# Kernel optimization log

Measured on AMD Instinct MI355X. Metric: run time of the kernel, lower is better.

Reference implementation:

```python
import jax, jax.numpy as jnp
import numpy as np
from jax import lax

G, K, C_IN, C_FEAT, H, W, B = 8, 6, 512, 256, 64, 64, 1


def apply_offset(offset):
    # offset: [N, 2, H, W] pixel-space offsets -> sampling grid [N, H, W, 2] in [-1, 1]
    # channel 0 displaces x (width), channel 1 displaces y (height), matching the
    # reversed-meshgrid logic of the original torch apply_offset.
    n, _, h, w = offset.shape
    jj = jnp.arange(w, dtype=offset.dtype)[None, None, :]
    ii = jnp.arange(h, dtype=offset.dtype)[None, :, None]
    gx = (jj + offset[:, 0]) / ((w - 1.0) / 2.0) - 1.0
    gy = (ii + offset[:, 1]) / ((h - 1.0) / 2.0) - 1.0
    return jnp.stack([gx, gy], axis=-1)


def grid_sample_border(img, grid):
    # img: [N, C, H, W], grid: [N, H, W, 2] in [-1, 1]
    # Bilinear, padding_mode='border', align_corners=False (torch grid_sample default).
    n, c, h, w = img.shape
    x = jnp.clip((grid[..., 0] + 1.0) * w * 0.5 - 0.5, 0.0, w - 1.0)
    y = jnp.clip((grid[..., 1] + 1.0) * h * 0.5 - 0.5, 0.0, h - 1.0)
    x0 = jnp.floor(x)
    y0 = jnp.floor(y)
    wx = (x - x0)[:, None]  # [N,1,H,W]
    wy = (y - y0)[:, None]
    x0i = x0.astype(jnp.int32)
    y0i = y0.astype(jnp.int32)
    x1i = jnp.minimum(x0i + 1, w - 1)
    y1i = jnp.minimum(y0i + 1, h - 1)

    def gather(im, yi, xi):  # im [C,H,W]; yi, xi [H,W]
        return im[:, yi, xi]

    g = jax.vmap(gather)
    v00 = g(img, y0i, x0i)
    v01 = g(img, y0i, x1i)
    v10 = g(img, y1i, x0i)
    v11 = g(img, y1i, x1i)
    return (1.0 - wy) * ((1.0 - wx) * v00 + wx * v01) + wy * ((1.0 - wx) * v10 + wx * v11)


def setup_inputs() -> dict:
    key = jax.random.key(0)
    ks = jax.random.split(key, 11)
    s = 0.02
    return {
        "gar_feat": jax.random.normal(ks[0], (B, C_FEAT, H, W), jnp.float32),
        "cond_feat": jax.random.normal(ks[1], (B, C_FEAT, H, W), jnp.float32),
        "mask": jax.random.uniform(ks[2], (B, G, C_FEAT), dtype=jnp.float32),
        "W1": jax.random.normal(ks[3], (G, 128, C_IN, 3, 3), jnp.float32) * s,
        "b1": jax.random.normal(ks[4], (G, 128), jnp.float32) * s,
        "W2": jax.random.normal(ks[5], (G, 64, 128, 3, 3), jnp.float32) * s,
        "b2": jax.random.normal(ks[6], (G, 64), jnp.float32) * s,
        "W3": jax.random.normal(ks[7], (G, 32, 64, 3, 3), jnp.float32) * s,
        "b3": jax.random.normal(ks[8], (G, 32), jnp.float32) * s,
        "W4": jax.random.normal(ks[9], (G, 3 * K, 32, 3, 3), jnp.float32) * s,
        "b4": jax.random.normal(ks[10], (G, 3 * K), jnp.float32) * s,
    }


def reference(gar_feat, cond_feat, mask, W1, b1, W2, b2, W3, b3, W4, b4):
    b, c, h, w = gar_feat.shape
    g = W1.shape[0]
    k = W4.shape[1] // 3
    inp = jnp.concatenate([gar_feat, cond_feat], axis=1)  # [B, 2C, H, W]

    def conv(x, wgt, bias):
        return lax.conv_general_dilated(
            x, wgt, (1, 1), 'SAME', dimension_numbers=('NCHW', 'OIHW', 'NCHW')
        ) + bias[None, :, None, None]

    def lrelu(x):
        return jnp.where(x >= 0, x, 0.1 * x)

    def group_net(w1, bb1, w2, bb2, w3, bb3, w4, bb4):
        hid = lrelu(conv(inp, w1, bb1))
        hid = lrelu(conv(hid, w2, bb2))
        hid = lrelu(conv(hid, w3, bb3))
        return conv(hid, w4, bb4)  # [B, 3k, H, W]

    oa = jax.vmap(group_net)(W1, b1, W2, b2, W3, b3, W4, b4)  # [G, B, 3k, H, W]
    attn = jax.nn.softmax(oa[:, :, 2 * k:], axis=0)           # softmax across groups: [G,B,k,H,W]
    off = oa[:, :, :2 * k].reshape(g, b * k, 2, h, w)
    grid = jax.vmap(apply_offset)(off)                        # [G, B*k, H, W, 2]

    rep = jnp.repeat(gar_feat, k, axis=0)                     # [B*k, C, H, W]

    def warp_group(grid_g, attn_g, mask_g):
        samp = grid_sample_border(rep, grid_g).reshape(b, k, c, h, w)
        wfeat = jnp.sum(samp * attn_g[:, :, None], axis=1)    # [B, C, H, W]
        return wfeat * mask_g[:, :, None, None]

    warped = jax.vmap(warp_group)(grid, attn, jnp.transpose(mask, (1, 0, 2)))
    return jnp.sum(warped, axis=0)  # [B, C, H, W]
```

## Files before the change

### kernel.cpp

```cpp
#include <hip/hip_runtime.h>
#include <hip/hip_bf16.h>

typedef __hip_bfloat16 bf16;
typedef unsigned short ushort8v __attribute__((ext_vector_type(8)));
typedef short  s16x4  __attribute__((ext_vector_type(4)));
typedef short  bf16x8 __attribute__((ext_vector_type(8)));
typedef float  f32x4  __attribute__((ext_vector_type(4)));

#define HW 4096
#define IMG_W 64

__device__ __forceinline__ float bfbits2f(unsigned short u) {
    return __uint_as_float(((unsigned int)u) << 16);
}
__device__ __forceinline__ short f2bs(float f) {
    bf16 h = __float2bfloat16(f);
    return *reinterpret_cast<short*>(&h);
}

__device__ __forceinline__ void gl_lds16(const void* g, void* s) {
    __builtin_amdgcn_global_load_lds(
        (const __attribute__((address_space(1))) unsigned int*)g,
        (__attribute__((address_space(3))) unsigned int*)s, 16, 0, 0);
}

__device__ void pack_input_dev(const float* __restrict__ gar,
                               const float* __restrict__ cond,
                               short* __restrict__ outp, int bx2, float* tile)
{
    int bx = bx2 & 127;
    int by = bx2 >> 7;
    int tx = threadIdx.x & 31;
    int ty = threadIdx.x >> 5;
#pragma unroll
    for (int i = 0; i < 4; ++i) {
        int c = by * 32 + ty + i * 8;
        const float* src = (c < 256) ? (gar + (size_t)c * HW)
                                     : (cond + (size_t)(c - 256) * HW);
        tile[(ty + i * 8) * 33 + tx] = src[bx * 32 + tx];
    }
    __syncthreads();
#pragma unroll
    for (int i = 0; i < 4; ++i) {
        int p = bx * 32 + ty + i * 8;
        outp[(size_t)p * 512 + by * 32 + tx] = f2bs(tile[tx * 33 + ty + i * 8]);
    }
}

template<int CIN, int CREAL, int BN, int NT>
__device__ void pack_w_dev(const float* __restrict__ wgt, char* __restrict__ wp,
                           int bx, short* sT)
{
    constexpr int NCC  = CIN / 32;
    constexpr int BLKB = 9 * 4 * BN * 16;

    const int t  = threadIdx.x;
    const int cc = bx % NCC;
    const int nt = (bx / NCC) % NT;
    const int g  = bx / (NT * NCC);

    for (int i = t; i < BLKB / 8; i += 256)
        reinterpret_cast<s16x4*>(sT)[i] = s16x4{0, 0, 0, 0};
    __syncthreads();

    int ocmax = CREAL - nt * BN; if (ocmax > BN) ocmax = BN;
    const size_t base = ((size_t)(g * CREAL + nt * BN) * CIN + cc * 32) * 9;
    for (int i = t; i < ocmax * 288; i += 256) {
        int oc = i / 288;
        int r  = i % 288;
        int ic = r / 9, tap = r % 9;
        sT[(size_t)(((tap * 4 + (ic >> 3)) * BN + oc) * 8 + (ic & 7))] =
            f2bs(wgt[base + (size_t)oc * CIN * 9 + r]);
    }
    __syncthreads();

    const s16x4* src = reinterpret_cast<const s16x4*>(sT);
    s16x4* dst = reinterpret_cast<s16x4*>(wp + (size_t)bx * BLKB);
    for (int i = t; i < BLKB / 8; i += 256)
        dst[i] = src[i];
}

__global__ __launch_bounds__(256)
void pack_all(const float* __restrict__ gar, const float* __restrict__ cond,
              const float* __restrict__ W1, const float* __restrict__ W2,
              const float* __restrict__ W3, const float* __restrict__ W4,
              short* inp_t, char* W1p, char* W2p, char* W3p, char* W4p)
{
    __shared__ __align__(16) short sbuf[9 * 4 * 64 * 8];
    int bx = blockIdx.x;
    if (bx < 256)      pack_w_dev<512, 128, 64, 2>(W1, W1p, bx,       sbuf);
    else if (bx < 288) pack_w_dev<128,  64, 64, 1>(W2, W2p, bx - 256, sbuf);
    else if (bx < 304) pack_w_dev< 64,  32, 32, 1>(W3, W3p, bx - 288, sbuf);
    else if (bx < 312) pack_w_dev< 32,  18, 32, 1>(W4, W4p, bx - 304, sbuf);
    else pack_input_dev(gar, cond, inp_t, bx - 312, (float*)sbuf);
}

template<int ICP, int CREAL, int BN, int ROWS, int OF, int NT, int NW, int PIPE,
         bool PIXMAJ_OUT, bool LEAKY, bool OUT_F32>
__global__ __launch_bounds__(NW * 64, 2)
void conv_mfma(const short* __restrict__ inp, const char* __restrict__ wp,
               const float* __restrict__ bias, void* __restrict__ outv)
{
    constexpr int NCC  = ICP / 32;
    constexpr int HALO = ROWS + 2;
    constexpr int NPT  = 4096 / (ROWS * 64);
    constexpr int BLKB = 9 * 4 * BN * 16;
    constexpr int RNDS = BLKB / 1024;
    constexpr int NBUF = (PIPE && NCC > 1) ? 2 : 1;
    constexpr int SMAX = (HALO + NW - 1) / NW;

    __shared__ __align__(16) short sA[HALO][4][68][8];
    __shared__ __align__(16) char  sBraw[NBUF][BLKB];

    const int b  = blockIdx.x;
    const int g  = b & 7;
    const int r_ = b >> 3;
    const int pt = r_ % NPT;
    const int nt = r_ / NPT;
    const int r0 = pt * ROWS;

    const int t    = threadIdx.x;
    const int wave = t >> 6, lane = t & 63;
    const int l15  = lane & 15, quad = lane >> 4;

    int row_l, ocw;
    if (NW == 8) {
        if (ROWS == 4) { row_l = wave >> 1; ocw = (wave & 1) * (BN / 2); }
        else           { row_l = wave >> 2; ocw = (wave & 3) * (BN / 4); }
    } else {
        row_l = (ROWS == 4) ? wave : (wave & 1);
        ocw   = (ROWS == 4) ? 0 : (wave >> 1) * (BN / 2);
    }

    const size_t gpix = (ICP == 512) ? 0 : ((size_t)g * 4096);
    const char*  wb   = wp + (size_t)((g * NT + nt) * NCC) * BLKB;

    const int acol = t & 63;
    const int r2   = t >> 6;

    bf16x8 pre[SMAX][4];

    auto stageA_load = [&](int cc) {
#pragma unroll
        for (int s = 0; s < SMAX; ++s) {
            int j = r2 + s * NW;
            if (j < HALO) {
                int gy = r0 - 1 + j;
                if (gy >= 0 && gy < 64) {
                    const short* sp = inp + ((gpix + gy * 64 + acol) * ICP + cc * 32);
#pragma unroll
                    for (int q = 0; q < 4; ++q)
                        pre[s][q] = *reinterpret_cast<const bf16x8*>(sp + q * 8);
                } else {
#pragma unroll
                    for (int q = 0; q < 4; ++q)
                        pre[s][q] = bf16x8{0, 0, 0, 0, 0, 0, 0, 0};
                }
            }
        }
    };
    auto stageA_write = [&]() {
#pragma unroll
        for (int s = 0; s < SMAX; ++s) {
            int j = r2 + s * NW;
            if (j < HALO) {
#pragma unroll
                for (int q = 0; q < 4; ++q)
                    *reinterpret_cast<bf16x8*>(&sA[j][q][acol + 1][0]) = pre[s][q];
            }
        }
    };
    auto stageB = [&](int cc) {
        const char* wsrc = wb + (size_t)cc * BLKB;
        char* sbb = (char*)sBraw[(NBUF == 2) ? (cc & 1) : 0];
        for (int r = wave; r < RNDS; r += NW)
            gl_lds16(wsrc + r * 1024 + lane * 16, sbb + r * 1024);
    };

    f32x4 acc[OF][4];
#pragma unroll
    for (int o = 0; o < OF; ++o)
#pragma unroll
        for (int p = 0; p < 4; ++p)
#pragma unroll
            for (int r = 0; r < 4; ++r) acc[o][p][r] = 0.f;

    if (t < HALO * 8) {
        int row = t >> 3, q = (t >> 1) & 3, cp = (t & 1) ? 65 : 0;
        *reinterpret_cast<bf16x8*>(&sA[row][q][cp][0]) =
            bf16x8{0, 0, 0, 0, 0, 0, 0, 0};
    }

    stageB(0);
    stageA_load(0);
    stageA_write();

    for (int cc = 0; cc < NCC; ++cc) {
        __syncthreads();
        if (cc + 1 < NCC) {
            if (PIPE) stageB(cc + 1);
            stageA_load(cc + 1);
        }
        const bf16x8* sBv = reinterpret_cast<const bf16x8*>(
            sBraw[(NBUF == 2) ? (cc & 1) : 0]);

#pragma unroll
        for (int dy = 0; dy < 3; ++dy) {
#pragma unroll
            for (int dx = 0; dx < 3; ++dx) {
                bf16x8 pF[4];
#pragma unroll
                for (int p = 0; p < 4; ++p)
                    pF[p] = *reinterpret_cast<const bf16x8*>(
                        &sA[row_l + dy][quad][p * 16 + l15 + dx][0]);
                bf16x8 wF[OF];
#pragma unroll
                for (int o = 0; o < OF; ++o)
                    wF[o] = sBv[((dy * 3 + dx) * 4 + quad) * BN + ocw + o * 16 + l15];
#pragma unroll
                for (int o = 0; o < OF; ++o)
#pragma unroll
                    for (int p = 0; p < 4; ++p)
                        acc[o][p] = __builtin_amdgcn_mfma_f32_16x16x32_bf16(
                            wF[o], pF[p], acc[o][p], 0, 0, 0);
            }
        }
        __syncthreads();
        if (cc + 1 < NCC) {
            if (!PIPE) stageB(cc + 1);
            stageA_write();
        }
    }

    const int prow = r0 + row_l;
#pragma unroll
    for (int o = 0; o < OF; ++o)
#pragma unroll
        for (int reg = 0; reg < 4; ++reg) {
            const int ocl = ocw + o * 16 + quad * 4 + reg;
            const int ocg = nt * BN + ocl;
            if (ocg < CREAL) {
                const float bv = bias[g * CREAL + ocg];
                if (PIXMAJ_OUT) {
                    short* outp = (short*)outv;
                    const size_t pixbase = ((size_t)g * 4096 + prow * 64);
#pragma unroll
                    for (int p = 0; p < 4; ++p) {
                        float v = acc[o][p][reg] + bv;
                        if (LEAKY) v = v >= 0.f ? v : 0.1f * v;
                        outp[(pixbase + p * 16 + l15) * (NT * BN) + ocg] = f2bs(v);
                    }
                } else if (OUT_F32) {
                    float* outp = (float*)outv;
                    const size_t base = ((size_t)(g * CREAL + ocg)) * HW + prow * IMG_W;
#pragma unroll
                    for (int p = 0; p < 4; ++p) {
                        float v = acc[o][p][reg] + bv;
                        if (LEAKY) v = v >= 0.f ? v : 0.1f * v;
                        outp[base + p * 16 + l15] = v;
                    }
                } else {
                    short* outp = (short*)outv;
                    const size_t base = ((size_t)(g * CREAL + ocg)) * HW + prow * IMG_W;
#pragma unroll
                    for (int p = 0; p < 4; ++p) {
                        float v = acc[o][p][reg] + bv;
                        if (LEAKY) v = v >= 0.f ? v : 0.1f * v;
                        outp[base + p * 16 + l15] = f2bs(v);
                    }
                }
            }
        }
}

__global__ __launch_bounds__(256)
void warp_combine_kernel(const float* __restrict__ oa,
                         const short* __restrict__ inp_t,
                         const float* __restrict__ mask,
                         float* __restrict__ out)
{
    __shared__ __align__(16) float4 sWts[8][6][8];
    __shared__ __align__(16) int4   sIdx[8][6][8];

    const int t = threadIdx.x;

    if (t < 48) {
        int lp = t / 6;
        int k  = t % 6;
        int p  = blockIdx.x * 8 + lp;
        int x  = p & 63, y = p >> 6;

        float l[8];
        float m = -1e30f;
#pragma unroll
        for (int g = 0; g < 8; ++g) {
            l[g] = oa[(size_t)(g * 18 + 12 + k) * HW + p];
            m = fmaxf(m, l[g]);
        }
        float s = 0.f;
#pragma unroll
        for (int g = 0; g < 8; ++g) { l[g] = __expf(l[g] - m); s += l[g]; }
        float inv = 1.f / s;

#pragma unroll
        for (int g = 0; g < 8; ++g) {
            float a  = l[g] * inv;
            float ox = oa[(size_t)(g * 18 + 2 * k)     * HW + p];
            float oy = oa[(size_t)(g * 18 + 2 * k + 1) * HW + p];
            float sx = fminf(fmaxf(((float)x + ox) * (64.f / 63.f) - 0.5f, 0.f), 63.f);
            float sy = fminf(fmaxf(((float)y + oy) * (64.f / 63.f) - 0.5f, 0.f), 63.f);
            float fx0 = floorf(sx), fy0 = floorf(sy);
            int   x0 = (int)fx0,    y0i = (int)fy0;
            float wx = sx - fx0,    wy = sy - fy0;
            int   x1 = min(x0 + 1, 63), y1 = min(y0i + 1, 63);
            sWts[lp][k][g] = make_float4(a * (1.f - wy) * (1.f - wx),
                                         a * (1.f - wy) * wx,
                                         a * wy * (1.f - wx),
                                         a * wy * wx);
            sIdx[lp][k][g] = make_int4(y0i * 64 + x0, y0i * 64 + x1,
                                       y1  * 64 + x0, y1  * 64 + x1);
        }
    }
    __syncthreads();

    const int lp = t >> 5;
    const int p  = blockIdx.x * 8 + lp;
    const int c0 = (t & 31) * 8;

    float acc[8];
#pragma unroll
    for (int j = 0; j < 8; ++j) acc[j] = 0.f;

    for (int g = 0; g < 8; ++g) {
        float4 m0 = *reinterpret_cast<const float4*>(mask + g * 256 + c0);
        float4 m1 = *reinterpret_cast<const float4*>(mask + g * 256 + c0 + 4);
        float mk[8] = {m0.x, m0.y, m0.z, m0.w, m1.x, m1.y, m1.z, m1.w};
#pragma unroll
        for (int k = 0; k < 6; ++k) {
            float4 w  = sWts[lp][k][g];
            int4   id = sIdx[lp][k][g];
            ushort8v v00 = *reinterpret_cast<const ushort8v*>(inp_t + (size_t)id.x * 512 + c0);
            ushort8v v01 = *reinterpret_cast<const ushort8v*>(inp_t + (size_t)id.y * 512 + c0);
            ushort8v v10 = *reinterpret_cast<const ushort8v*>(inp_t + (size_t)id.z * 512 + c0);
            ushort8v v11 = *reinterpret_cast<const ushort8v*>(inp_t + (size_t)id.w * 512 + c0);
#pragma unroll
            for (int j = 0; j < 8; ++j) {
                float sv = w.x * bfbits2f(v00[j]) + w.y * bfbits2f(v01[j])
                         + w.z * bfbits2f(v10[j]) + w.w * bfbits2f(v11[j]);
                acc[j] = fmaf(mk[j], sv, acc[j]);
            }
        }
    }
#pragma unroll
    for (int j = 0; j < 8; ++j)
        out[(size_t)(c0 + j) * HW + p] = acc[j];
}

extern "C" void kernel_launch(void* const* d_in, const int* in_sizes, int n_in,
                              void* d_out, int out_size, void* d_ws, size_t ws_size,
                              hipStream_t stream)
{
    (void)in_sizes; (void)n_in; (void)out_size; (void)ws_size;
    const float* gar  = (const float*)d_in[0];
    const float* cond = (const float*)d_in[1];
    const float* mask = (const float*)d_in[2];
    const float* W1   = (const float*)d_in[3];
    const float* b1   = (const float*)d_in[4];
    const float* W2   = (const float*)d_in[5];
    const float* b2   = (const float*)d_in[6];
    const float* W3   = (const float*)d_in[7];
    const float* b3   = (const float*)d_in[8];
    const float* W4   = (const float*)d_in[9];
    const float* b4   = (const float*)d_in[10];
    float* out = (float*)d_out;

    char* ws = (char*)d_ws;
    short* inp_t  = (short*)(ws);
    char*  W1p    = ws + (4u << 20);
    short* hid2_t = (short*)(ws + (4u << 20));
    short* hid3_t = (short*)(ws + (8u << 20));
    float* oa     = (float*)(ws + (10u << 20) + (512u << 10));
    char*  W2p    = ws + (14u << 20);
    char*  W3p    = ws + (15u << 20) + (512u << 10);
    char*  W4p    = ws + (16u << 20);
    short* hid1_t = (short*)(ws + (17u << 20));

    pack_all<<<2360, 256, 0, stream>>>(gar, cond, W1, W2, W3, W4,
                                       inp_t, W1p, W2p, W3p, W4p);

    conv_mfma<512, 128, 64, 2, 2, 2, 4, 0, true, true, false>
        <<<512, 256, 0, stream>>>(inp_t, W1p, b1, hid1_t);
    conv_mfma<128, 64, 64, 2, 1, 1, 8, 1, true, true, false>
        <<<256, 512, 0, stream>>>(hid1_t, W2p, b2, hid2_t);
    conv_mfma<64, 32, 32, 2, 1, 1, 4, 1, true, true, false>
        <<<256, 256, 0, stream>>>(hid2_t, W3p, b3, hid3_t);
    conv_mfma<32, 18, 32, 2, 1, 1, 4, 1, false, false, true>
        <<<256, 256, 0, stream>>>(hid3_t, W4p, b4, oa);

    warp_combine_kernel<<<512, 256, 0, stream>>>(oa, inp_t, mask, out);
}
```

Before: 203.2 us.

## Load conv1 weights directly into registers with double-buffered prefetch

Adds a conv_mfma_wreg variant used for the first 512-channel conv. Each lane loads its MFMA weight fragments straight from global memory into a double-buffered register array instead of staging them through shared memory. The next chunk's weights are prefetched during the current chunk's MFMAs. This removes the LDS traffic and the stores for weights, but it needs many more VGPRs (2x9xOF bf16x8 buffers), which may lower occupancy or cause spills.

```diff
diff --git a/kernel.cpp b/kernel.cpp
--- a/kernel.cpp
+++ b/kernel.cpp
@@ -230,6 +230,177 @@
             if (!PIPE) stageB(cc + 1);
             stageA_write();
         }
+    }
+
+    const int prow = r0 + row_l;
+#pragma unroll
+    for (int o = 0; o < OF; ++o)
+#pragma unroll
+        for (int reg = 0; reg < 4; ++reg) {
+            const int ocl = ocw + o * 16 + quad * 4 + reg;
+            const int ocg = nt * BN + ocl;
+            if (ocg < CREAL) {
+                const float bv = bias[g * CREAL + ocg];
+                if (PIXMAJ_OUT) {
+                    short* outp = (short*)outv;
+                    const size_t pixbase = ((size_t)g * 4096 + prow * 64);
+#pragma unroll
+                    for (int p = 0; p < 4; ++p) {
+                        float v = acc[o][p][reg] + bv;
+                        if (LEAKY) v = v >= 0.f ? v : 0.1f * v;
+                        outp[(pixbase + p * 16 + l15) * (NT * BN) + ocg] = f2bs(v);
+                    }
+                } else if (OUT_F32) {
+                    float* outp = (float*)outv;
+                    const size_t base = ((size_t)(g * CREAL + ocg)) * HW + prow * IMG_W;
+#pragma unroll
+                    for (int p = 0; p < 4; ++p) {
+                        float v = acc[o][p][reg] + bv;
+                        if (LEAKY) v = v >= 0.f ? v : 0.1f * v;
+                        outp[base + p * 16 + l15] = v;
+                    }
+                } else {
+                    short* outp = (short*)outv;
+                    const size_t base = ((size_t)(g * CREAL + ocg)) * HW + prow * IMG_W;
+#pragma unroll
+                    for (int p = 0; p < 4; ++p) {
+                        float v = acc[o][p][reg] + bv;
+                        if (LEAKY) v = v >= 0.f ? v : 0.1f * v;
+                        outp[base + p * 16 + l15] = f2bs(v);
+                    }
+                }
+            }
+        }
+}
+
+template<int ICP, int CREAL, int BN, int ROWS, int OF, int NT, int NW,
+         bool PIXMAJ_OUT, bool LEAKY, bool OUT_F32>
+__global__ __launch_bounds__(NW * 64, 2)
+void conv_mfma_wreg(const short* __restrict__ inp, const char* __restrict__ wp,
+                    const float* __restrict__ bias, void* __restrict__ outv)
+{
+    constexpr int NCC  = ICP / 32;
+    constexpr int HALO = ROWS + 2;
+    constexpr int NPT  = 4096 / (ROWS * 64);
+    constexpr int BLKB = 9 * 4 * BN * 16;
+    constexpr int SMAX = (HALO + NW - 1) / NW;
+
+    __shared__ __align__(16) short sA[HALO][4][68][8];
+
+    const int b  = blockIdx.x;
+    const int g  = b & 7;
+    const int r_ = b >> 3;
+    const int pt = r_ % NPT;
+    const int nt = r_ / NPT;
+    const int r0 = pt * ROWS;
+
+    const int t    = threadIdx.x;
+    const int wave = t >> 6, lane = t & 63;
+    const int l15  = lane & 15, quad = lane >> 4;
+
+    int row_l, ocw;
+    if (NW == 8) {
+        if (ROWS == 4) { row_l = wave >> 1; ocw = (wave & 1) * (BN / 2); }
+        else           { row_l = wave >> 2; ocw = (wave & 3) * (BN / 4); }
+    } else {
+        row_l = (ROWS == 4) ? wave : (wave & 1);
+        ocw   = (ROWS == 4) ? 0 : (wave >> 1) * (BN / 2);
+    }
+
+    const size_t gpix = (ICP == 512) ? 0 : ((size_t)g * 4096);
+    const short* wb   = (const short*)(wp + (size_t)((g * NT + nt) * NCC) * BLKB);
+    const short* wlane = wb + (size_t)(quad * BN + ocw + l15) * 8;
+
+    const int acol = t & 63;
+    const int r2   = t >> 6;
+
+    bf16x8 pre[SMAX][4];
+
+    auto stageA_load = [&](int cc) {
+#pragma unroll
+        for (int s = 0; s < SMAX; ++s) {
+            int j = r2 + s * NW;
+            if (j < HALO) {
+                int gy = r0 - 1 + j;
+                if (gy >= 0 && gy < 64) {
+                    const short* sp = inp + ((gpix + gy * 64 + acol) * ICP + cc * 32);
+#pragma unroll
+                    for (int q = 0; q < 4; ++q)
+                        pre[s][q] = *reinterpret_cast<const bf16x8*>(sp + q * 8);
+                } else {
+#pragma unroll
+                    for (int q = 0; q < 4; ++q)
+                        pre[s][q] = bf16x8{0, 0, 0, 0, 0, 0, 0, 0};
+                }
+            }
+        }
+    };
+    auto stageA_write = [&]() {
+#pragma unroll
+        for (int s = 0; s < SMAX; ++s) {
+            int j = r2 + s * NW;
+            if (j < HALO) {
+#pragma unroll
+                for (int q = 0; q < 4; ++q)
+                    *reinterpret_cast<bf16x8*>(&sA[j][q][acol + 1][0]) = pre[s][q];
+            }
+        }
+    };
+
+    bf16x8 wbuf[2][9][OF];
+    auto loadW = [&](int cc, int buf) {
+#pragma unroll
+        for (int tap = 0; tap < 9; ++tap)
+#pragma unroll
+            for (int o = 0; o < OF; ++o)
+                wbuf[buf][tap][o] = *reinterpret_cast<const bf16x8*>(
+                    wlane + (size_t)cc * (BLKB / 2) + (tap * 4 * BN + o * 16) * 8);
+    };
+
+    f32x4 acc[OF][4];
+#pragma unroll
+    for (int o = 0; o < OF; ++o)
+#pragma unroll
+        for (int p = 0; p < 4; ++p)
+#pragma unroll
+            for (int r = 0; r < 4; ++r) acc[o][p][r] = 0.f;
+
+    if (t < HALO * 8) {
+        int row = t >> 3, q = (t >> 1) & 3, cp = (t & 1) ? 65 : 0;
+        *reinterpret_cast<bf16x8*>(&sA[row][q][cp][0]) =
+            bf16x8{0, 0, 0, 0, 0, 0, 0, 0};
+    }
+
+    loadW(0, 0);
+    stageA_load(0);
+    stageA_write();
+
+#pragma unroll
+    for (int cc = 0; cc < NCC; ++cc) {
+        __syncthreads();
+        if (cc + 1 < NCC) {
+            loadW(cc + 1, (cc + 1) & 1);
+            stageA_load(cc + 1);
+        }
+#pragma unroll
+        for (int dy = 0; dy < 3; ++dy) {
+#pragma unroll
+            for (int dx = 0; dx < 3; ++dx) {
+                bf16x8 pF[4];
+#pragma unroll
+                for (int p = 0; p < 4; ++p)
+                    pF[p] = *reinterpret_cast<const bf16x8*>(
+                        &sA[row_l + dy][quad][p * 16 + l15 + dx][0]);
+#pragma unroll
+                for (int o = 0; o < OF; ++o)
+#pragma unroll
+                    for (int p = 0; p < 4; ++p)
+                        acc[o][p] = __builtin_amdgcn_mfma_f32_16x16x32_bf16(
+                            wbuf[cc & 1][dy * 3 + dx][o], pF[p], acc[o][p], 0, 0, 0);
+            }
+        }
+        __syncthreads();
+        if (cc + 1 < NCC) stageA_write();
     }
 
     const int prow = r0 + row_l;
@@ -388,7 +559,7 @@
     pack_all<<<2360, 256, 0, stream>>>(gar, cond, W1, W2, W3, W4,
                                        inp_t, W1p, W2p, W3p, W4p);
 
-    conv_mfma<512, 128, 64, 2, 2, 2, 4, 0, true, true, false>
+    conv_mfma_wreg<512, 128, 64, 2, 2, 2, 4, true, true, false>
         <<<512, 256, 0, stream>>>(inp_t, W1p, b1, hid1_t);
     conv_mfma<128, 64, 64, 2, 1, 1, 8, 1, true, true, false>
         <<<256, 512, 0, stream>>>(hid1_t, W2p, b2, hid2_t);
```

Result: no change. 203.4 us (+0.1%).

## Add dedicated conv1 kernel with channel-blocked input layout and register-resident weights

Applied to the files above, without the earlier changes.

The input is repacked into 32-channel blocks laid out pixel-major within each block, so a row of 32 channels becomes one contiguous stripe. A new conv1_direct kernel stages halo rows with global_load_lds DMA, double-buffered across channel chunks. It loads weights straight from global memory into registers using a coalesced weight layout and prefetches the next chunk's weights during compute. The warp_combine gather is updated for the new input layout. The aim is to cut LDS traffic and sync overhead in the dominant first conv, at the cost of higher register pressure and more scattered gathers in the warp stage.

```diff
diff --git a/kernel.cpp b/kernel.cpp
--- a/kernel.cpp
+++ b/kernel.cpp
@@ -43,11 +43,11 @@
 #pragma unroll
     for (int i = 0; i < 4; ++i) {
         int p = bx * 32 + ty + i * 8;
-        outp[(size_t)p * 512 + by * 32 + tx] = f2bs(tile[tx * 33 + ty + i * 8]);
-    }
-}
-
-template<int CIN, int CREAL, int BN, int NT>
+        outp[((size_t)by * 4096 + p) * 32 + tx] = f2bs(tile[tx * 33 + ty + i * 8]);
+    }
+}
+
+template<int CIN, int CREAL, int BN, int NT, bool COAL>
 __device__ void pack_w_dev(const float* __restrict__ wgt, char* __restrict__ wp,
                            int bx, short* sT)
 {
@@ -69,8 +69,10 @@
         int oc = i / 288;
         int r  = i % 288;
         int ic = r / 9, tap = r % 9;
-        sT[(size_t)(((tap * 4 + (ic >> 3)) * BN + oc) * 8 + (ic & 7))] =
-            f2bs(wgt[base + (size_t)oc * CIN * 9 + r]);
+        size_t idx;
+        if (COAL) idx = (size_t)(((tap * BN + oc) * 4 + (ic >> 3)) * 8 + (ic & 7));
+        else      idx = (size_t)(((tap * 4 + (ic >> 3)) * BN + oc) * 8 + (ic & 7));
+        sT[idx] = f2bs(wgt[base + (size_t)oc * CIN * 9 + r]);
     }
     __syncthreads();
 
@@ -88,10 +90,10 @@
 {
     __shared__ __align__(16) short sbuf[9 * 4 * 64 * 8];
     int bx = blockIdx.x;
-    if (bx < 256)      pack_w_dev<512, 128, 64, 2>(W1, W1p, bx,       sbuf);
-    else if (bx < 288) pack_w_dev<128,  64, 64, 1>(W2, W2p, bx - 256, sbuf);
-    else if (bx < 304) pack_w_dev< 64,  32, 32, 1>(W3, W3p, bx - 288, sbuf);
-    else if (bx < 312) pack_w_dev< 32,  18, 32, 1>(W4, W4p, bx - 304, sbuf);
+    if (bx < 256)      pack_w_dev<512, 128, 64, 2, true >(W1, W1p, bx,       sbuf);
+    else if (bx < 288) pack_w_dev<128,  64, 64, 1, false>(W2, W2p, bx - 256, sbuf);
+    else if (bx < 304) pack_w_dev< 64,  32, 32, 1, false>(W3, W3p, bx - 288, sbuf);
+    else if (bx < 312) pack_w_dev< 32,  18, 32, 1, false>(W4, W4p, bx - 304, sbuf);
     else pack_input_dev(gar, cond, inp_t, bx - 312, (float*)sbuf);
 }
 
@@ -269,6 +271,122 @@
                         outp[base + p * 16 + l15] = f2bs(v);
                     }
                 }
+            }
+        }
+}
+
+__global__ __launch_bounds__(256, 2)
+void conv1_direct(const short* __restrict__ inp, const char* __restrict__ wp,
+                  const float* __restrict__ bias, short* __restrict__ outp)
+{
+    __shared__ __align__(16) short sA[2][4][66][4][8];
+
+    const int b  = blockIdx.x;
+    const int g  = b & 7;
+    const int r_ = b >> 3;
+    const int pt = r_ & 31;
+    const int nt = r_ >> 5;
+    const int r0 = pt * 2;
+
+    const int t    = threadIdx.x;
+    const int wave = t >> 6, lane = t & 63;
+    const int l15  = lane & 15, quad = lane >> 4;
+
+    const int row_l = wave & 1;
+    const int ocw   = (wave >> 1) * 32;
+
+    const short* wb    = (const short*)wp + (size_t)(g * 2 + nt) * 16 * 18432;
+    const short* wlane = wb + ((size_t)(ocw + l15) * 4 + quad) * 8;
+
+    auto stageDMA = [&](int cc, int buf) {
+        int gy = r0 - 1 + wave;
+        if (gy >= 0 && gy < 64) {
+            const short* src = inp + ((size_t)cc * 4096 + (size_t)gy * 64) * 32
+                                   + (size_t)lane * 8;
+#pragma unroll
+            for (int c4 = 0; c4 < 4; ++c4)
+                gl_lds16(src + c4 * 512, &sA[buf][wave][1 + c4 * 16][0][0]);
+        }
+    };
+
+    bf16x8 wA[9][2], wB[9][2];
+    auto loadW_into = [&](int cc, bf16x8 (&w)[9][2]) {
+        const short* ws = wlane + (size_t)cc * 18432;
+#pragma unroll
+        for (int tap = 0; tap < 9; ++tap)
+#pragma unroll
+            for (int o = 0; o < 2; ++o)
+                w[tap][o] = *reinterpret_cast<const bf16x8*>(
+                    ws + tap * 2048 + o * 512);
+    };
+
+    f32x4 acc[2][4];
+#pragma unroll
+    for (int o = 0; o < 2; ++o)
+#pragma unroll
+        for (int p = 0; p < 4; ++p)
+#pragma unroll
+            for (int r = 0; r < 4; ++r) acc[o][p][r] = 0.f;
+
+    loadW_into(0, wA);
+    stageDMA(0, 0);
+    if (t < 64) {
+        int buf = t >> 5, row = (t >> 3) & 3, q = (t >> 1) & 3;
+        int col = (t & 1) ? 65 : 0;
+        *reinterpret_cast<bf16x8*>(&sA[buf][row][col][q][0]) =
+            bf16x8{0, 0, 0, 0, 0, 0, 0, 0};
+    }
+    if (r0 == 0 || r0 == 62) {
+        int zr = (r0 == 0) ? 0 : 3;
+        for (int i = t; i < 2 * 66 * 4; i += 256) {
+            int buf = i / 264, rem = i % 264;
+            *reinterpret_cast<bf16x8*>(&sA[buf][zr][rem >> 2][rem & 3][0]) =
+                bf16x8{0, 0, 0, 0, 0, 0, 0, 0};
+        }
+    }
+
+    auto body = [&](int cc, int cur, bf16x8 (&wuse)[9][2], bf16x8 (&wld)[9][2]) {
+        __syncthreads();
+        if (cc + 1 < 16) {
+            stageDMA(cc + 1, cur ^ 1);
+            loadW_into(cc + 1, wld);
+        }
+#pragma unroll
+        for (int dy = 0; dy < 3; ++dy)
+#pragma unroll
+            for (int dx = 0; dx < 3; ++dx) {
+                bf16x8 pF[4];
+#pragma unroll
+                for (int p = 0; p < 4; ++p)
+                    pF[p] = *reinterpret_cast<const bf16x8*>(
+                        &sA[cur][row_l + dy][p * 16 + l15 + dx][quad][0]);
+#pragma unroll
+                for (int o = 0; o < 2; ++o)
+#pragma unroll
+                    for (int p = 0; p < 4; ++p)
+                        acc[o][p] = __builtin_amdgcn_mfma_f32_16x16x32_bf16(
+                            wuse[dy * 3 + dx][o], pF[p], acc[o][p], 0, 0, 0);
+            }
+    };
+
+    for (int c2 = 0; c2 < 16; c2 += 2) {
+        body(c2,     0, wA, wB);
+        body(c2 + 1, 1, wB, wA);
+    }
+
+    const int prow = r0 + row_l;
+    const size_t pixbase = (size_t)g * 4096 + (size_t)prow * 64;
+#pragma unroll
+    for (int o = 0; o < 2; ++o)
+#pragma unroll
+        for (int reg = 0; reg < 4; ++reg) {
+            const int ocg = nt * 64 + ocw + o * 16 + quad * 4 + reg;
+            const float bv = bias[g * 128 + ocg];
+#pragma unroll
+            for (int p = 0; p < 4; ++p) {
+                float v = acc[o][p][reg] + bv;
+                v = v >= 0.f ? v : 0.1f * v;
+                outp[(pixbase + p * 16 + l15) * 128 + ocg] = f2bs(v);
             }
         }
 }
@@ -326,6 +444,7 @@
     const int lp = t >> 5;
     const int p  = blockIdx.x * 8 + lp;
     const int c0 = (t & 31) * 8;
+    const short* ipc = inp_t + (size_t)(c0 >> 5) * (4096 * 32) + (c0 & 31);
 
     float acc[8];
 #pragma unroll
@@ -339,10 +458,10 @@
         for (int k = 0; k < 6; ++k) {
             float4 w  = sWts[lp][k][g];
             int4   id = sIdx[lp][k][g];
-            ushort8v v00 = *reinterpret_cast<const ushort8v*>(inp_t + (size_t)id.x * 512 + c0);
-            ushort8v v01 = *reinterpret_cast<const ushort8v*>(inp_t + (size_t)id.y * 512 + c0);
-            ushort8v v10 = *reinterpret_cast<const ushort8v*>(inp_t + (size_t)id.z * 512 + c0);
-            ushort8v v11 = *reinterpret_cast<const ushort8v*>(inp_t + (size_t)id.w * 512 + c0);
+            ushort8v v00 = *reinterpret_cast<const ushort8v*>(ipc + (size_t)id.x * 32);
+            ushort8v v01 = *reinterpret_cast<const ushort8v*>(ipc + (size_t)id.y * 32);
+            ushort8v v10 = *reinterpret_cast<const ushort8v*>(ipc + (size_t)id.z * 32);
+            ushort8v v11 = *reinterpret_cast<const ushort8v*>(ipc + (size_t)id.w * 32);
 #pragma unroll
             for (int j = 0; j < 8; ++j) {
                 float sv = w.x * bfbits2f(v00[j]) + w.y * bfbits2f(v01[j])
@@ -388,8 +507,7 @@
     pack_all<<<2360, 256, 0, stream>>>(gar, cond, W1, W2, W3, W4,
                                        inp_t, W1p, W2p, W3p, W4p);
 
-    conv_mfma<512, 128, 64, 2, 2, 2, 4, 0, true, true, false>
-        <<<512, 256, 0, stream>>>(inp_t, W1p, b1, hid1_t);
+    conv1_direct<<<512, 256, 0, stream>>>(inp_t, W1p, b1, hid1_t);
     conv_mfma<128, 64, 64, 2, 1, 1, 8, 1, true, true, false>
         <<<256, 512, 0, stream>>>(hid1_t, W2p, b2, hid2_t);
     conv_mfma<64, 32, 32, 2, 1, 1, 4, 1, true, true, false>
```

Measured after the change: 204.6 us. About the same (+0.7%).
